# Optimization experiments

Hardware: AMD Instinct MI355X
Metric: run time of the kernel (lower is better)

The kernel has to match this reference:

```python
import jax, jax.numpy as jnp
import numpy as np

WIDTH = 4096
NUM_HEADS = 8
BLOCK_W = WIDTH // NUM_HEADS


def _block_diag_linear(x, w, b):
    # x: [n, width] -> [n, h, bw]; w: [h, bw, bw]; b: [h, bw]
    n = x.shape[0]
    xh = x.reshape(n, NUM_HEADS, BLOCK_W)
    y = jnp.einsum('nhi,hij->nhj', xh, w) + b
    return y.reshape(n, WIDTH)


def setup_inputs() -> dict:
    key = jax.random.key(0)
    ks = jax.random.split(key, 7)
    n = 8192
    x = jax.random.normal(ks[0], (n, WIDTH), dtype=jnp.float32)
    s = jnp.sort(jax.random.randint(ks[1], (n,), 0, 8, dtype=jnp.int32))
    # a_param init: uniform on ring radii [0.9, 0.999], softplus-inverse transform
    eps = 1e-8
    u = jax.random.uniform(ks[2], (WIDTH,), minval=0.9**2 + eps, maxval=0.999**2 + eps)
    t = 0.5 * jnp.log(u)
    a_param = jnp.log(jnp.exp(-t) - 1.0).astype(jnp.float32)
    std = 1.0 / np.sqrt(BLOCK_W)
    ig_w = std * jax.random.normal(ks[3], (NUM_HEADS, BLOCK_W, BLOCK_W), dtype=jnp.float32)
    ig_b = jnp.zeros((NUM_HEADS, BLOCK_W), dtype=jnp.float32)
    ag_w = std * jax.random.normal(ks[4], (NUM_HEADS, BLOCK_W, BLOCK_W), dtype=jnp.float32)
    ag_b = jnp.zeros((NUM_HEADS, BLOCK_W), dtype=jnp.float32)
    return {'x': x, 's': s, 'a_param': a_param, 'ig_w': ig_w, 'ig_b': ig_b,
            'ag_w': ag_w, 'ag_b': ag_b}


def reference(x, s, a_param, ig_w, ig_b, ag_w, ag_b):
    n, k = x.shape
    # reset mask: True at position 0 and wherever segment id changes
    reset = jnp.concatenate([jnp.ones((1,), dtype=bool), s[1:] != s[:-1]])
    gate_x = jax.nn.sigmoid(_block_diag_linear(x, ig_w, ig_b))
    gate_a = jax.nn.sigmoid(_block_diag_linear(x, ag_w, ag_b))
    log_a = -8.0 * gate_a * jax.nn.softplus(a_param)  # [n, k]
    a = jnp.exp(log_a)
    a_square = jnp.exp(2.0 * log_a)
    multiplier = jnp.sqrt(1.0 - a_square)
    multiplier = jnp.where(reset[:, None], 1.0, multiplier)
    normalized_x = x * gate_x * multiplier
    # linear recurrence h[t] = a[t] * h[t-1] + normalized_x[t] via parallel scan
    def combine(e1, e2):
        a1, b1 = e1
        a2, b2 = e2
        return (a1 * a2, a2 * b1 + b2)
    _, out = jax.lax.associative_scan(combine, (a, normalized_x), axis=0)
    return out
```

## Files before the change

kernel.cpp:

```cpp
#include <hip/hip_runtime.h>
#include <hip/hip_bf16.h>
#include <stdint.h>

#define WIDTH 4096
#define NROWS 8192
#define NHEADS 8
#define BW 512
#define CS 128
#define NCHUNK (NROWS/CS)
#define LOG2E 1.4426950408889634f

typedef short bf16x8 __attribute__((ext_vector_type(8)));
typedef float f32x4 __attribute__((ext_vector_type(4)));

__device__ __forceinline__ uint32_t rne_bf16(float f) {
  uint32_t u = __float_as_uint(f);
  return (u + 0x7fffu + ((u >> 16) & 1u)) >> 16;
}
__device__ __forceinline__ float bf16_to_f32(uint32_t bits) {
  return __uint_as_float(bits << 16);
}
__device__ __forceinline__ uint32_t cvtpk(float a, float b) {
  uint32_t r;
  asm("v_cvt_pk_bf16_f32 %0, %1, %2" : "=v"(r) : "v"(a), "v"(b));
  return r;
}

__device__ __forceinline__ void gload_lds16(const void* g, void* l) {
  __builtin_amdgcn_global_load_lds(
      (const __attribute__((address_space(1))) void*)g,
      (__attribute__((address_space(3))) void*)l, 16, 0, 0);
}

__global__ void prep_all(const float* __restrict__ x, uint16_t* __restrict__ xb,
                         const float* __restrict__ ig_w, const float* __restrict__ ag_w,
                         uint16_t* __restrict__ wt,
                         const float* __restrict__ a_param, float* __restrict__ cvec2) {
  __shared__ float tile[32][33];
  const int b = blockIdx.x;
  const int tid = threadIdx.x;
  if (b < 4096) {
    int m  = b >> 8;
    int j0 = ((b >> 4) & 15) * 32;
    int i0 = (b & 15) * 32;
    const float* src = ((m >> 3) ? ag_w : ig_w) + (size_t)(m & 7) * BW * BW;
    int tx = tid & 31, ty = tid >> 5;
    #pragma unroll
    for (int k = 0; k < 4; k++) {
      int i = i0 + ty + 8 * k;
      tile[ty + 8 * k][tx] = src[(size_t)i * BW + (j0 + tx)] * LOG2E;
    }
    __syncthreads();
    #pragma unroll
    for (int k = 0; k < 4; k++) {
      int j = j0 + ty + 8 * k;
      wt[((size_t)m * BW + j) * BW + (i0 + tx)] = (uint16_t)rne_bf16(tile[tx][ty + 8 * k]);
    }
  } else if (b < 6144) {
    int bb = b - 4096;
    #pragma unroll
    for (int it = 0; it < 8; it++) {
      size_t i = (((size_t)it * 2048 + bb) * 256 + tid) * 8;
      float4 f0 = *reinterpret_cast<const float4*>(x + i);
      float4 f1 = *reinterpret_cast<const float4*>(x + i + 4);
      uint4 v;
      v.x = cvtpk(f0.x, f0.y); v.y = cvtpk(f0.z, f0.w);
      v.z = cvtpk(f1.x, f1.y); v.w = cvtpk(f1.z, f1.w);
      *reinterpret_cast<uint4*>(xb + i) = v;
    }
  } else {
    int i = (b - 6144) * 256 + tid;
    if (i < WIDTH) {
      float v = a_param[i];
      float sp = (v > 15.f) ? v : log1pf(expf(v));
      cvec2[i] = 8.f * sp * LOG2E;
    }
  }
}

#define BM 128
#define BN 64
#define BK 32

__global__ __launch_bounds__(256, 4)
void gates_gemm(const uint16_t* __restrict__ xb,
                const int* __restrict__ s,
                const uint16_t* __restrict__ wt,
                const float* __restrict__ ig_b,
                const float* __restrict__ ag_b,
                const float* __restrict__ cvec2,
                uint32_t* __restrict__ lanx,
                float* __restrict__ cA,
                float* __restrict__ cB) {
  __shared__ __align__(16) unsigned char dsm[32768];
  __shared__ unsigned char resetm[BM];

  const int b = blockIdx.x;
  const int orig = (b & 7) * 512 + (b >> 3);
  const int h  = orig >> 9;
  const int rem = orig & 511;
  const int mt = rem >> 3;
  const int nt = rem & 7;
  const int m0 = mt * BM;
  const int j0 = nt * BN;

  const int tid = threadIdx.x;
  const int lane = tid & 63;
  const int w = tid >> 6;
  const int wr = w >> 1;
  const int wc = w & 1;
  const int lrow = lane & 15;
  const int lkg  = lane >> 4;

  if (tid < BM) {
    int n = m0 + tid;
    resetm[tid] = (n == 0) || (s[n] != s[n - 1]);
  }

  const char* xb_src[2];
  #pragma unroll
  for (int i = 0; i < 2; i++) {
    int o = i * 4096 + tid * 16;
    int row = o >> 6;
    int cc = o & 63;
    int cbyte = ((((cc >> 4) ^ ((row >> 1) & 3)) << 4)) | (cc & 15);
    xb_src[i] = (const char*)xb + (size_t)(m0 + row) * (WIDTH * 2) + h * (BW * 2) + cbyte;
  }
  const char* w_src[2];
  #pragma unroll
  for (int i = 0; i < 2; i++) {
    int o = i * 4096 + tid * 16;
    int g = o >> 12;
    int jl = (o >> 6) & 63;
    int cc = o & 63;
    int cbyte = ((((cc >> 4) ^ ((jl >> 1) & 3)) << 4)) | (cc & 15);
    w_src[i] = (const char*)wt + ((size_t)((g * 8 + h) * BW + (j0 + jl))) * (BW * 2) + cbyte;
  }

  f32x4 acc[2][4][2];
  #pragma unroll
  for (int g = 0; g < 2; g++)
    #pragma unroll
    for (int mf = 0; mf < 4; mf++)
      #pragma unroll
      for (int nf = 0; nf < 2; nf++)
        acc[g][mf][nf] = (f32x4){0.f, 0.f, 0.f, 0.f};

  {
    const int p0 = (2 * nt + 2) & 15;
    #pragma unroll
    for (int i = 0; i < 2; i++)
      gload_lds16(xb_src[i] + p0 * 64, dsm + i * 4096 + tid * 16);
    #pragma unroll
    for (int i = 0; i < 2; i++)
      gload_lds16(w_src[i] + p0 * 64, dsm + 8192 + i * 4096 + tid * 16);
  }
  __syncthreads();

  for (int st = 0; st < 16; st++) {
    const uint32_t bufb = (uint32_t)(st & 1) << 14;
    if (st < 15) {
      const uint32_t nb = bufb ^ 16384u;
      const int p = (2 * nt + 3 + st) & 15;
      #pragma unroll
      for (int i = 0; i < 2; i++)
        gload_lds16(xb_src[i] + p * 64, dsm + nb + i * 4096 + tid * 16);
      #pragma unroll
      for (int i = 0; i < 2; i++)
        gload_lds16(w_src[i] + p * 64, dsm + nb + 8192 + i * 4096 + tid * 16);
    }
    bf16x8 af[4];
    #pragma unroll
    for (int mf = 0; mf < 4; mf++) {
      int row = wr * 64 + 16 * mf + lrow;
      uint32_t addr = bufb + (uint32_t)(row << 6)
                    + (uint32_t)((lkg << 4) ^ (((row >> 1) & 3) << 4));
      af[mf] = *reinterpret_cast<const bf16x8*>(dsm + addr);
    }
    __builtin_amdgcn_s_setprio(1);
    #pragma unroll
    for (int g = 0; g < 2; g++) {
      #pragma unroll
      for (int nf = 0; nf < 2; nf++) {
        int j = wc * 32 + 16 * nf + lrow;
        uint32_t addr = bufb + 8192u + (uint32_t)(g << 12) + (uint32_t)(j << 6)
                      + (uint32_t)((lkg << 4) ^ (((j >> 1) & 3) << 4));
        bf16x8 bfr = *reinterpret_cast<const bf16x8*>(dsm + addr);
        #pragma unroll
        for (int mf = 0; mf < 4; mf++) {
          acc[g][mf][nf] = __builtin_amdgcn_mfma_f32_16x16x32_bf16(
              af[mf], bfr, acc[g][mf][nf], 0, 0, 0);
        }
      }
    }
    __builtin_amdgcn_s_setprio(0);
    __syncthreads();
  }

  float* smf = (float*)(dsm + 8192);

  const int jl0 = wc * 32 + lrow;
  float igb[2], agb[2], cv2[2];
  #pragma unroll
  for (int nf = 0; nf < 2; nf++) {
    int jj = h * BW + j0 + jl0 + 16 * nf;
    igb[nf] = ig_b[jj] * LOG2E; agb[nf] = ag_b[jj] * LOG2E; cv2[nf] = cvec2[jj];
  }

  float segA[2][4], segB[2][4];
  #pragma unroll
  for (int mf = 0; mf < 4; mf++) {
    float A[2] = {1.f, 1.f}, B[2] = {0.f, 0.f};
    int rbase = wr * 64 + 16 * mf + 4 * lkg;
    #pragma unroll
    for (int r = 0; r < 4; r++) {
      int row = rbase + r;
      int n = m0 + row;
      bool rs = resetm[row] != 0;
      uint32_t xsw = (uint32_t)(((row >> 1) & 3) << 4);
      #pragma unroll
      for (int nf = 0; nf < 2; nf++) {
        int jl = jl0 + 16 * nf;
        size_t o = (size_t)n * WIDTH + h * BW + j0 + jl;
        float yig = acc[0][mf][nf][r] + igb[nf];
        float yag = acc[1][mf][nf][r] + agb[nf];
        float gx = __builtin_amdgcn_rcpf(1.f + exp2f(-yig));
        float ga = __builtin_amdgcn_rcpf(1.f + exp2f(-yag));
        float la2 = -ga * cv2[nf];
        float la_r = bf16_to_f32(cvtpk(la2, la2) & 0xffffu);
        float a = exp2f(la_r);
        float mult = rs ? 1.f
                     : __builtin_amdgcn_sqrtf(fmaxf(1.f - a * a, 0.f));
        int cb = (jl & 31) * 2;
        uint32_t xaddr = ((jl >> 5) ? 16384u : 0u) + (uint32_t)(row << 6)
                       + (uint32_t)(((uint32_t)(cb >> 4) << 4) ^ xsw) + (uint32_t)(cb & 15);
        float xv = bf16_to_f32(*reinterpret_cast<const uint16_t*>(dsm + xaddr));
        float nx = xv * gx * mult;
        uint32_t word = cvtpk(la_r, nx);
        float nx_r = __uint_as_float(word & 0xffff0000u);
        lanx[o] = word;
        A[nf] *= a;
        B[nf] = fmaf(a, B[nf], nx_r);
      }
    }
    segA[0][mf] = A[0]; segB[0][mf] = B[0];
    segA[1][mf] = A[1]; segB[1][mf] = B[1];
  }
  #pragma unroll
  for (int nf = 0; nf < 2; nf++) {
    #pragma unroll
    for (int mf = 0; mf < 4; mf++) {
      float A = segA[nf][mf], B = segB[nf][mf];
      #pragma unroll
      for (int d = 16; d <= 32; d <<= 1) {
        float pA = __shfl_xor(A, d, 64);
        float pB = __shfl_xor(B, d, 64);
        bool up = (lane & d) != 0;
        B = up ? fmaf(A, pB, B) : fmaf(pA, B, pB);
        A *= pA;
      }
      segA[nf][mf] = A; segB[nf][mf] = B;
    }
    float colA = segA[nf][0], colB = segB[nf][0];
    #pragma unroll
    for (int mf = 1; mf < 4; mf++) {
      colB = fmaf(segA[nf][mf], colB, segB[nf][mf]);
      colA *= segA[nf][mf];
    }
    if (lkg == 0) {
      int clocal = wc * 32 + 16 * nf + lrow;
      smf[wr * 64 + clocal] = colA;
      smf[128 + wr * 64 + clocal] = colB;
    }
  }
  __syncthreads();
  if (tid < BN) {
    float A0 = smf[tid],       B0 = smf[128 + tid];
    float A1 = smf[64 + tid],  B1 = smf[192 + tid];
    float Af = A0 * A1;
    float Bf = fmaf(A1, B0, B1);
    int jj = h * BW + j0 + tid;
    cA[mt * WIDTH + jj] = Af;
    cB[mt * WIDTH + jj] = Bf;
  }
}

__global__ void scan_apply(const uint32_t* __restrict__ lanx,
                           const float* __restrict__ cA,
                           const float* __restrict__ cB,
                           float* __restrict__ out) {
  int chunk = blockIdx.x;
  int c0 = (blockIdx.y * 256 + threadIdx.x) * 4;
  size_t base = (size_t)chunk * CS * WIDTH + c0;
  float h[4] = {0.f, 0.f, 0.f, 0.f};
  for (int i = 0; i < chunk; i++) {
    float4 av = *reinterpret_cast<const float4*>(cA + i * WIDTH + c0);
    float4 bv = *reinterpret_cast<const float4*>(cB + i * WIDTH + c0);
    h[0] = fmaf(av.x, h[0], bv.x);
    h[1] = fmaf(av.y, h[1], bv.y);
    h[2] = fmaf(av.z, h[2], bv.z);
    h[3] = fmaf(av.w, h[3], bv.w);
  }
  for (int rb = 0; rb < CS; rb += 4) {
    uint4 v[4];
    #pragma unroll
    for (int e = 0; e < 4; e++)
      v[e] = *reinterpret_cast<const uint4*>(lanx + base + (size_t)(rb + e) * WIDTH);
    #pragma unroll
    for (int e = 0; e < 4; e++) {
      float4 ov;
      h[0] = fmaf(exp2f(bf16_to_f32(v[e].x & 0xffffu)), h[0], bf16_to_f32(v[e].x >> 16)); ov.x = h[0];
      h[1] = fmaf(exp2f(bf16_to_f32(v[e].y & 0xffffu)), h[1], bf16_to_f32(v[e].y >> 16)); ov.y = h[1];
      h[2] = fmaf(exp2f(bf16_to_f32(v[e].z & 0xffffu)), h[2], bf16_to_f32(v[e].z >> 16)); ov.z = h[2];
      h[3] = fmaf(exp2f(bf16_to_f32(v[e].w & 0xffffu)), h[3], bf16_to_f32(v[e].w >> 16)); ov.w = h[3];
      *reinterpret_cast<float4*>(out + base + (size_t)(rb + e) * WIDTH) = ov;
    }
  }
}

extern "C" void kernel_launch(void* const* d_in, const int* in_sizes, int n_in,
                              void* d_out, int out_size, void* d_ws, size_t ws_size,
                              hipStream_t stream) {
  const float* x       = (const float*)d_in[0];
  const int*   s       = (const int*)d_in[1];
  const float* a_param = (const float*)d_in[2];
  const float* ig_w    = (const float*)d_in[3];
  const float* ig_b    = (const float*)d_in[4];
  const float* ag_w    = (const float*)d_in[5];
  const float* ag_b    = (const float*)d_in[6];
  float* out = (float*)d_out;
  char* ws = (char*)d_ws;

  uint32_t* lanx   = (uint32_t*)ws;
  uint16_t* wt     = (uint16_t*)(ws + 134217728);
  uint16_t* xb     = (uint16_t*)(ws + 142606336);
  float*    cvec2  = (float*)(ws + 209715200);
  float*    cA     = (float*)(ws + 209731584);
  float*    cB     = (float*)(ws + 210780160);

  prep_all<<<dim3(6160), 256, 0, stream>>>(x, xb, ig_w, ag_w, wt, a_param, cvec2);
  gates_gemm<<<dim3(4096), 256, 0, stream>>>(xb, s, wt, ig_b, ag_b, cvec2,
                                             lanx, cA, cB);
  scan_apply<<<dim3(NCHUNK, 4), 256, 0, stream>>>(lanx, cA, cB, out);
}
```

Measured before the change: 224.8 us.

## Precompute chunk-carry prefixes in separate kernel; flatten x bf16 conversion grid

Adds a scan_prefix kernel that computes, once per column, the carried state entering each chunk. Previously every scan_apply block replayed all earlier chunk aggregates, which was quadratic redundant work and uneven across chunks. scan_apply now loads one prefix value per column. The x-to-bf16 conversion in prep_all also changes from 2048 blocks looping 8 times to 8192 blocks each handling 16 elements. The trade-off is an extra small, low-parallelism kernel launch (16 blocks, serial over 64 chunks) and an additional workspace buffer.

```diff
diff --git a/kernel.cpp b/kernel.cpp
--- a/kernel.cpp
+++ b/kernel.cpp
@@ -56,20 +56,21 @@
       int j = j0 + ty + 8 * k;
       wt[((size_t)m * BW + j) * BW + (i0 + tx)] = (uint16_t)rne_bf16(tile[tx][ty + 8 * k]);
     }
-  } else if (b < 6144) {
-    int bb = b - 4096;
-    #pragma unroll
-    for (int it = 0; it < 8; it++) {
-      size_t i = (((size_t)it * 2048 + bb) * 256 + tid) * 8;
-      float4 f0 = *reinterpret_cast<const float4*>(x + i);
-      float4 f1 = *reinterpret_cast<const float4*>(x + i + 4);
-      uint4 v;
-      v.x = cvtpk(f0.x, f0.y); v.y = cvtpk(f0.z, f0.w);
-      v.z = cvtpk(f1.x, f1.y); v.w = cvtpk(f1.z, f1.w);
-      *reinterpret_cast<uint4*>(xb + i) = v;
-    }
+  } else if (b < 12288) {
+    size_t i = ((size_t)(b - 4096) * 256 + tid) * 16;
+    float4 f0 = *reinterpret_cast<const float4*>(x + i);
+    float4 f1 = *reinterpret_cast<const float4*>(x + i + 4);
+    float4 f2 = *reinterpret_cast<const float4*>(x + i + 8);
+    float4 f3 = *reinterpret_cast<const float4*>(x + i + 12);
+    uint4 v0, v1;
+    v0.x = cvtpk(f0.x, f0.y); v0.y = cvtpk(f0.z, f0.w);
+    v0.z = cvtpk(f1.x, f1.y); v0.w = cvtpk(f1.z, f1.w);
+    v1.x = cvtpk(f2.x, f2.y); v1.y = cvtpk(f2.z, f2.w);
+    v1.z = cvtpk(f3.x, f3.y); v1.w = cvtpk(f3.z, f3.w);
+    *reinterpret_cast<uint4*>(xb + i) = v0;
+    *reinterpret_cast<uint4*>(xb + i + 8) = v1;
   } else {
-    int i = (b - 6144) * 256 + tid;
+    int i = (b - 12288) * 256 + tid;
     if (i < WIDTH) {
       float v = a_param[i];
       float sp = (v > 15.f) ? v : log1pf(expf(v));
@@ -285,22 +286,28 @@
   }
 }
 
+__global__ void scan_prefix(const float* __restrict__ cA, const float* __restrict__ cB,
+                            float* __restrict__ prefix) {
+  int c = blockIdx.x * 256 + threadIdx.x;
+  float hcur = 0.f;
+  for (int i0 = 0; i0 < NCHUNK; i0 += 8) {
+    float av[8], bv[8];
+    #pragma unroll
+    for (int e = 0; e < 8; e++) { av[e] = cA[(i0 + e) * WIDTH + c]; bv[e] = cB[(i0 + e) * WIDTH + c]; }
+    #pragma unroll
+    for (int e = 0; e < 8; e++) { prefix[(i0 + e) * WIDTH + c] = hcur; hcur = av[e] * hcur + bv[e]; }
+  }
+}
+
 __global__ void scan_apply(const uint32_t* __restrict__ lanx,
-                           const float* __restrict__ cA,
-                           const float* __restrict__ cB,
+                           const float* __restrict__ prefix,
                            float* __restrict__ out) {
   int chunk = blockIdx.x;
   int c0 = (blockIdx.y * 256 + threadIdx.x) * 4;
   size_t base = (size_t)chunk * CS * WIDTH + c0;
-  float h[4] = {0.f, 0.f, 0.f, 0.f};
-  for (int i = 0; i < chunk; i++) {
-    float4 av = *reinterpret_cast<const float4*>(cA + i * WIDTH + c0);
-    float4 bv = *reinterpret_cast<const float4*>(cB + i * WIDTH + c0);
-    h[0] = fmaf(av.x, h[0], bv.x);
-    h[1] = fmaf(av.y, h[1], bv.y);
-    h[2] = fmaf(av.z, h[2], bv.z);
-    h[3] = fmaf(av.w, h[3], bv.w);
-  }
+  float h[4];
+  #pragma unroll
+  for (int q = 0; q < 4; q++) h[q] = prefix[chunk * WIDTH + c0 + q];
   for (int rb = 0; rb < CS; rb += 4) {
     uint4 v[4];
     #pragma unroll
@@ -337,9 +344,11 @@
   float*    cvec2  = (float*)(ws + 209715200);
   float*    cA     = (float*)(ws + 209731584);
   float*    cB     = (float*)(ws + 210780160);
-
-  prep_all<<<dim3(6160), 256, 0, stream>>>(x, xb, ig_w, ag_w, wt, a_param, cvec2);
+  float*    prefix = (float*)(ws + 211828736);
+
+  prep_all<<<dim3(12304), 256, 0, stream>>>(x, xb, ig_w, ag_w, wt, a_param, cvec2);
   gates_gemm<<<dim3(4096), 256, 0, stream>>>(xb, s, wt, ig_b, ag_b, cvec2,
                                              lanx, cA, cB);
-  scan_apply<<<dim3(NCHUNK, 4), 256, 0, stream>>>(lanx, cA, cB, out);
-}
+  scan_prefix<<<dim3(16), 256, 0, stream>>>(cA, cB, prefix);
+  scan_apply<<<dim3(NCHUNK, 4), 256, 0, stream>>>(lanx, prefix, out);
+}
```

Result: faster. 207.1 us (-7.9%).
